# Optimization experiments

Hardware: AMD Instinct MI355X
Metric: run time of the kernel (lower is better)

## Reference

```python
import jax, jax.numpy as jnp
import numpy as np

N_ATOMS = 51200
N_MOL = 512
FEAT = 384


def setup_inputs() -> dict:
    key = jax.random.key(0)
    ks = jax.random.split(key, 20)
    s = 0.05  # small random weights instead of the degenerate zero-init
    inp = {
        "node_feats": jax.random.normal(ks[0], (N_ATOMS, FEAT), jnp.float32),
        "energy": jax.random.normal(ks[1], (N_MOL,), jnp.float32),
        "forces": jax.random.normal(ks[2], (N_ATOMS, 3), jnp.float32),
        "stress": jax.random.normal(ks[3], (N_MOL, 3, 3), jnp.float32),
        "W1": jax.random.normal(ks[4], (64, 256), jnp.float32) * s,
        "b1": jnp.zeros((64,), jnp.float32),
        "W2": jax.random.normal(ks[5], (16, 64), jnp.float32) * s,
        "b2": jnp.zeros((16,), jnp.float32),
        "W3": jax.random.normal(ks[6], (1, 16), jnp.float32) * s,
        "b3": jnp.zeros((1,), jnp.float32),
        "W1f": jax.random.normal(ks[7], (64, 256), jnp.float32) * s,
        "b1f": jnp.zeros((64,), jnp.float32),
        "W2f": jax.random.normal(ks[8], (16, 64), jnp.float32) * s,
        "b2f": jnp.zeros((16,), jnp.float32),
        "W3f": jax.random.normal(ks[9], (1, 16), jnp.float32) * s,
        "b3f": jnp.zeros((1,), jnp.float32),
        "S_uncert": jnp.zeros((1,), jnp.float32),
        # atom -> molecule segment ids (sorted, every molecule non-empty)
        "batch_idx": jnp.repeat(jnp.arange(N_MOL, dtype=jnp.int64), N_ATOMS // N_MOL),
    }
    return inp


def _mlp(x, W1, b1, W2, b2, W3, b3):
    h = jax.nn.silu(x @ W1.T + b1)
    h = jax.nn.silu(h @ W2.T + b2)
    return h @ W3.T + b3  # [N, 1]


def reference(node_feats, energy, forces, stress,
              W1, b1, W2, b2, W3, b3,
              W1f, b1f, W2f, b2f, W3f, b3f,
              S_uncert, batch_idx):
    # concat first 128 and last 128 feature channels -> [N, 256]
    nf = jnp.concatenate([node_feats[:, :128], node_feats[:, -128:]], axis=1)

    # E head: faithfully zeroed out and replaced by constant 0.6
    e_stds = jnp.exp(_mlp(nf, W1, b1, W2, b2, W3, b3))[:, 0] * 0 + 0.6  # [N]
    # F head
    f_u = jnp.exp(_mlp(nf, W1f, b1f, W2f, b2f, W3f, b3f))[:, 0] * 0.1   # [N]
    force_uncert = jnp.stack([f_u, f_u, f_u], axis=-1)                  # [N, 3]
    # stress uncert: constant 0.1/16 (S_uncert term zeroed, kept faithfully)
    stress_uncert = jnp.ones_like(stress) * jnp.exp(S_uncert[0]) * 0 + 0.1 / 16

    # per-molecule mean of e_stds via segment sums (scatter_add in torch)
    eu_sum = jax.ops.segment_sum(e_stds, batch_idx, num_segments=N_MOL)
    n_atoms = jax.ops.segment_sum(jnp.ones_like(e_stds), batch_idx, num_segments=N_MOL)
    energy_uncert = eu_sum / n_atoms  # [n_mol]

    return (energy, forces, stress, energy_uncert, force_uncert, stress_uncert)
```

## Files before the change

kernel.cpp:

```cpp
#include <hip/hip_runtime.h>
#include <hip/hip_bf16.h>

#define N_ATOMS 51200

#define OUT_FUNC 159232

typedef __attribute__((ext_vector_type(4))) float f32x4;
typedef __attribute__((ext_vector_type(2))) unsigned u32x2;
typedef __attribute__((ext_vector_type(4))) unsigned u32x4;
typedef __attribute__((ext_vector_type(8))) short s16x8;

constexpr int BLK = 256;

__device__ __forceinline__ unsigned pack2(float lo, float hi) {
    return __builtin_amdgcn_perm(__float_as_uint(hi), __float_as_uint(lo), 0x07060302);
}
__device__ __forceinline__ s16x8 pack8(f32x4 lo, f32x4 hi) {
    union { u32x4 u; s16x8 s; } c;
    c.u.x = pack2(lo.x, lo.y); c.u.y = pack2(lo.z, lo.w);
    c.u.z = pack2(hi.x, hi.y); c.u.w = pack2(hi.z, hi.w);
    return c.s;
}
__device__ __forceinline__ short bftrunc(float x) {
    return (short)(__float_as_uint(x) >> 16);
}
__device__ __forceinline__ float silu_(float v) { return v / (1.0f + __expf(-v)); }

__global__ __launch_bounds__(BLK, 4) void funcert_kernel(
    const float* __restrict__ nf,
    const float* __restrict__ energy,
    const float* __restrict__ forces,
    const float* __restrict__ stress,
    const float* __restrict__ W1f, const float* __restrict__ b1f,
    const float* __restrict__ W2f, const float* __restrict__ b2f,
    const float* __restrict__ W3f, const float* __restrict__ b3f,
    float* __restrict__ out)
{
    const int t   = threadIdx.x;
    const int gid = blockIdx.x * BLK + t;

    __shared__ short Xq[2][64 * 64];
    __shared__ short H1s[64 * 64];

    const int lane  = t & 63;
    const int w     = t >> 6;
    const int g     = lane >> 4;
    const int col   = lane & 15;
    const int abase = blockIdx.x * 64;
    const int ch    = w * 16 + col;

    const int rb  = t >> 4;
    const int f4c = t & 15;
    const float4* nfr = (const float4*)nf + (size_t)(abase + rb) * 96 + f4c;
    const int wbyte0 = rb * 128 + (f4c & 1) * 8;

    #define XQ_ISSUE(dst, qb)                                            \
        { _Pragma("unroll")                                              \
          for (int i = 0; i < 4; ++i)                                    \
              dst[i] = *(const f32x4*)(nfr + (size_t)i * 16 * 96 + (qb)); }

    #define XQ_STASH(buf, src)                                           \
        { _Pragma("unroll")                                              \
          for (int i = 0; i < 4; ++i) {                                  \
              const int r = rb + 16 * i;                                 \
              u32x2 bb;                                                  \
              bb.x = pack2(src[i].x, src[i].y);                          \
              bb.y = pack2(src[i].z, src[i].w);                          \
              *(u32x2*)((char*)(buf) + (wbyte0 + 2048 * i +              \
                        ((((f4c >> 1) ^ (r & 7))) << 4))) = bb;          \
          } }

    #define WQ_ISSUE(dst, q)                                             \
        { _Pragma("unroll")                                              \
          for (int ks2 = 0; ks2 < 2; ++ks2) {                            \
              const float* p = W1f + ch * 256 + (q) * 64 + ks2 * 32 + g * 8; \
              dst[2 * ks2]     = *(const f32x4*)p;                       \
              dst[2 * ks2 + 1] = *(const f32x4*)(p + 4);                 \
          } }

    #define Q_COMPUTE(buf, wf)                                           \
        { _Pragma("unroll")                                              \
          for (int mt = 0; mt < 4; ++mt) {                               \
              const int row = mt * 16 + col;                             \
              _Pragma("unroll")                                          \
              for (int ks2 = 0; ks2 < 2; ++ks2) {                        \
                  const int sl = (ks2 * 4 + g) ^ (row & 7);              \
                  const s16x8 af = *(const s16x8*)((buf) + row * 64 + sl * 8); \
                  acc[mt] = __builtin_amdgcn_mfma_f32_16x16x32_bf16(af, wf[ks2], acc[mt], 0, 0, 0); \
              } } }

    f32x4 cv = {0.f, 0.f, 0.f, 0.f}; int co = -1;
    if (gid < 40960) {
        co = gid;
        if      (gid < 128)   { cv = ((const f32x4*)energy)[gid]; }
        else if (gid < 38528) { cv = ((const f32x4*)forces)[gid - 128]; }
        else if (gid < 39680) { cv = ((const f32x4*)stress)[gid - 38528]; }
        else if (gid < 39808) { cv = (f32x4){0.6f, 0.6f, 0.6f, 0.6f}; }
        else { cv = (f32x4){0.00625f, 0.00625f, 0.00625f, 0.00625f}; co = gid + 38400; }
    }

    f32x4 wv[4];
    WQ_ISSUE(wv, 0);
    const float b1v = b1f[ch];
    f32x4 xa[4], xb[4], xc[4];
    XQ_ISSUE(xa, 0);
    XQ_ISSUE(xb, 16);
    XQ_ISSUE(xc, 64);

    f32x4 acc[4];
    #pragma unroll
    for (int mt = 0; mt < 4; ++mt) acc[mt] = (f32x4){0.f, 0.f, 0.f, 0.f};
    s16x8 wf[2];

    wf[0] = pack8(wv[0], wv[1]); wf[1] = pack8(wv[2], wv[3]);
    XQ_STASH(Xq[0], xa);
    __syncthreads();
    WQ_ISSUE(wv, 1);
    XQ_ISSUE(xa, 80);
    Q_COMPUTE(Xq[0], wf);
    __syncthreads();

    wf[0] = pack8(wv[0], wv[1]); wf[1] = pack8(wv[2], wv[3]);
    XQ_STASH(Xq[1], xb);
    __syncthreads();
    WQ_ISSUE(wv, 2);
    Q_COMPUTE(Xq[1], wf);
    __syncthreads();

    wf[0] = pack8(wv[0], wv[1]); wf[1] = pack8(wv[2], wv[3]);
    XQ_STASH(Xq[0], xc);
    __syncthreads();
    WQ_ISSUE(wv, 3);
    Q_COMPUTE(Xq[0], wf);
    __syncthreads();

    wf[0] = pack8(wv[0], wv[1]); wf[1] = pack8(wv[2], wv[3]);
    XQ_STASH(Xq[1], xa);
    __syncthreads();
    Q_COMPUTE(Xq[1], wf);

    #pragma unroll
    for (int mt = 0; mt < 4; ++mt) {
        #pragma unroll
        for (int r = 0; r < 4; ++r) {
            const int atom = mt * 16 + g * 4 + r;
            H1s[atom * 64 + ch] = bftrunc(silu_(acc[mt][r] + b1v));
        }
    }
    __syncthreads();

    s16x8 w2frag[2];
    #pragma unroll
    for (int ks = 0; ks < 2; ++ks) {
        const float* p = W2f + col * 64 + ks * 32 + g * 8;
        w2frag[ks] = pack8(*(const f32x4*)p, *(const f32x4*)(p + 4));
    }
    const int arow = w * 16 + col;
    f32x4 a2 = {0.f, 0.f, 0.f, 0.f};
    #pragma unroll
    for (int ks = 0; ks < 2; ++ks) {
        const s16x8 af = *(const s16x8*)(H1s + arow * 64 + ks * 32 + g * 8);
        a2 = __builtin_amdgcn_mfma_f32_16x16x32_bf16(af, w2frag[ks], a2, 0, 0, 0);
    }

    const float b2v = b2f[col];
    const float w3v = W3f[col];
    float y[4];
    #pragma unroll
    for (int r = 0; r < 4; ++r)
        y[r] = silu_(a2[r] + b2v) * w3v;
    #pragma unroll
    for (int m = 1; m < 16; m <<= 1) {
        #pragma unroll
        for (int r = 0; r < 4; ++r)
            y[r] += __shfl_xor(y[r], m, 64);
    }
    const float b3v = b3f[0];
    float fu[4];
    #pragma unroll
    for (int r = 0; r < 4; ++r)
        fu[r] = __expf(y[r] + b3v) * 0.1f;

    if (col < 12) {
        const int a_ = col / 3, c = col - a_ * 3;
        const float v = (a_ == 0) ? fu[0] : (a_ == 1) ? fu[1] : (a_ == 2) ? fu[2] : fu[3];
        const int atom = w * 16 + g * 4 + a_;
        out[OUT_FUNC + 3 * (abase + atom) + c] = v;
    }

    if (co >= 0) ((f32x4*)out)[co] = cv;
}

extern "C" void kernel_launch(void* const* d_in, const int* in_sizes, int n_in,
                              void* d_out, int out_size, void* d_ws, size_t ws_size,
                              hipStream_t stream) {
    const float* nf     = (const float*)d_in[0];
    const float* energy = (const float*)d_in[1];
    const float* forces = (const float*)d_in[2];
    const float* stress = (const float*)d_in[3];
    const float* W1f    = (const float*)d_in[10];
    const float* b1f    = (const float*)d_in[11];
    const float* W2f    = (const float*)d_in[12];
    const float* b2f    = (const float*)d_in[13];
    const float* W3f    = (const float*)d_in[14];
    const float* b3f    = (const float*)d_in[15];
    float* out = (float*)d_out;

    dim3 grid(N_ATOMS / 64);
    funcert_kernel<<<grid, BLK, 0, stream>>>(nf, energy, forces, stress,
                                             W1f, b1f, W2f, b2f, W3f, b3f, out);
}
```

Measured before the change: 20.69 us.

## Stage node features into LDS via direct global_load_lds in fp32

Replaces the register-staged path for node feature tiles with asynchronous global-to-LDS loads. Before, tiles were loaded to registers, packed to bf16 and stored to LDS. The tiles now stay fp32 in LDS, in an XOR-swizzled layout, and are converted to bf16 only when building MFMA operands. This removes the intermediate registers and one barrier per stage, reducing VGPR pressure and instruction count. The cost is a doubled LDS footprint for the double buffer and a shallower prefetch, which may limit occupancy or latency hiding.

```diff
diff --git a/kernel.cpp b/kernel.cpp
--- a/kernel.cpp
+++ b/kernel.cpp
@@ -6,7 +6,6 @@
 #define OUT_FUNC 159232
 
 typedef __attribute__((ext_vector_type(4))) float f32x4;
-typedef __attribute__((ext_vector_type(2))) unsigned u32x2;
 typedef __attribute__((ext_vector_type(4))) unsigned u32x4;
 typedef __attribute__((ext_vector_type(8))) short s16x8;
 
@@ -39,7 +38,7 @@
     const int t   = threadIdx.x;
     const int gid = blockIdx.x * BLK + t;
 
-    __shared__ short Xq[2][64 * 64];
+    __shared__ float Xq[2][64 * 64];
     __shared__ short H1s[64 * 64];
 
     const int lane  = t & 63;
@@ -49,44 +48,43 @@
     const int abase = blockIdx.x * 64;
     const int ch    = w * 16 + col;
 
-    const int rb  = t >> 4;
-    const int f4c = t & 15;
-    const float4* nfr = (const float4*)nf + (size_t)(abase + rb) * 96 + f4c;
-    const int wbyte0 = rb * 128 + (f4c & 1) * 8;
-
-    #define XQ_ISSUE(dst, qb)                                            \
-        { _Pragma("unroll")                                              \
-          for (int i = 0; i < 4; ++i)                                    \
-              dst[i] = *(const f32x4*)(nfr + (size_t)i * 16 * 96 + (qb)); }
-
-    #define XQ_STASH(buf, src)                                           \
-        { _Pragma("unroll")                                              \
-          for (int i = 0; i < 4; ++i) {                                  \
-              const int r = rb + 16 * i;                                 \
-              u32x2 bb;                                                  \
-              bb.x = pack2(src[i].x, src[i].y);                          \
-              bb.y = pack2(src[i].z, src[i].w);                          \
-              *(u32x2*)((char*)(buf) + (wbyte0 + 2048 * i +              \
-                        ((((f4c >> 1) ^ (r & 7))) << 4))) = bb;          \
+    const int rloc = lane >> 4;
+    const int sl   = lane & 15;
+
+    #define GLD_Q(b, qf)                                                     \
+        { _Pragma("unroll")                                                  \
+          for (int i2 = 0; i2 < 4; ++i2) {                                   \
+              const int ii = w * 4 + i2;                                     \
+              const int r  = 4 * ii + rloc;                                  \
+              const int c  = sl ^ ((r & 7) << 1);                            \
+              const float* src = nf + (size_t)(abase + r) * 384 + (qf) + c * 4; \
+              __builtin_amdgcn_global_load_lds(                              \
+                  (const __attribute__((address_space(1))) void*)src,        \
+                  (__attribute__((address_space(3))) void*)(&Xq[b][ii * 256]), \
+                  16, 0, 0);                                                 \
           } }
 
-    #define WQ_ISSUE(dst, q)                                             \
-        { _Pragma("unroll")                                              \
-          for (int ks2 = 0; ks2 < 2; ++ks2) {                            \
+    #define WQ_ISSUE(dst, q)                                                 \
+        { _Pragma("unroll")                                                  \
+          for (int ks2 = 0; ks2 < 2; ++ks2) {                                \
               const float* p = W1f + ch * 256 + (q) * 64 + ks2 * 32 + g * 8; \
-              dst[2 * ks2]     = *(const f32x4*)p;                       \
-              dst[2 * ks2 + 1] = *(const f32x4*)(p + 4);                 \
+              dst[2 * ks2]     = *(const f32x4*)p;                           \
+              dst[2 * ks2 + 1] = *(const f32x4*)(p + 4);                     \
           } }
 
-    #define Q_COMPUTE(buf, wf)                                           \
-        { _Pragma("unroll")                                              \
-          for (int mt = 0; mt < 4; ++mt) {                               \
-              const int row = mt * 16 + col;                             \
-              _Pragma("unroll")                                          \
-              for (int ks2 = 0; ks2 < 2; ++ks2) {                        \
-                  const int sl = (ks2 * 4 + g) ^ (row & 7);              \
-                  const s16x8 af = *(const s16x8*)((buf) + row * 64 + sl * 8); \
-                  acc[mt] = __builtin_amdgcn_mfma_f32_16x16x32_bf16(af, wf[ks2], acc[mt], 0, 0, 0); \
+    #define Q_COMPUTE(b, wfv)                                                \
+        { _Pragma("unroll")                                                  \
+          for (int mt = 0; mt < 4; ++mt) {                                   \
+              const int row = mt * 16 + col;                                 \
+              const int xr  = (row & 7) << 1;                                \
+              _Pragma("unroll")                                              \
+              for (int ks2 = 0; ks2 < 2; ++ks2) {                            \
+                  const int s0 = ((ks2 << 3) + (g << 1)) ^ xr;               \
+                  const float* p = &Xq[b][row * 64 + s0 * 4];                \
+                  const f32x4 lo = *(const f32x4*)p;                         \
+                  const f32x4 hi = *(const f32x4*)(p + 4);                   \
+                  acc[mt] = __builtin_amdgcn_mfma_f32_16x16x32_bf16(         \
+                              pack8(lo, hi), wfv[ks2], acc[mt], 0, 0, 0);    \
               } } }
 
     f32x4 cv = {0.f, 0.f, 0.f, 0.f}; int co = -1;
@@ -102,42 +100,35 @@
     f32x4 wv[4];
     WQ_ISSUE(wv, 0);
     const float b1v = b1f[ch];
-    f32x4 xa[4], xb[4], xc[4];
-    XQ_ISSUE(xa, 0);
-    XQ_ISSUE(xb, 16);
-    XQ_ISSUE(xc, 64);
+    GLD_Q(0, 0);
+
+    s16x8 wf[2];
+    wf[0] = pack8(wv[0], wv[1]); wf[1] = pack8(wv[2], wv[3]);
 
     f32x4 acc[4];
     #pragma unroll
     for (int mt = 0; mt < 4; ++mt) acc[mt] = (f32x4){0.f, 0.f, 0.f, 0.f};
-    s16x8 wf[2];
-
-    wf[0] = pack8(wv[0], wv[1]); wf[1] = pack8(wv[2], wv[3]);
-    XQ_STASH(Xq[0], xa);
+
     __syncthreads();
     WQ_ISSUE(wv, 1);
-    XQ_ISSUE(xa, 80);
-    Q_COMPUTE(Xq[0], wf);
-    __syncthreads();
-
-    wf[0] = pack8(wv[0], wv[1]); wf[1] = pack8(wv[2], wv[3]);
-    XQ_STASH(Xq[1], xb);
-    __syncthreads();
+    GLD_Q(1, 64);
+    Q_COMPUTE(0, wf);
+    __syncthreads();
+
+    wf[0] = pack8(wv[0], wv[1]); wf[1] = pack8(wv[2], wv[3]);
     WQ_ISSUE(wv, 2);
-    Q_COMPUTE(Xq[1], wf);
-    __syncthreads();
-
-    wf[0] = pack8(wv[0], wv[1]); wf[1] = pack8(wv[2], wv[3]);
-    XQ_STASH(Xq[0], xc);
-    __syncthreads();
+    GLD_Q(0, 256);
+    Q_COMPUTE(1, wf);
+    __syncthreads();
+
+    wf[0] = pack8(wv[0], wv[1]); wf[1] = pack8(wv[2], wv[3]);
     WQ_ISSUE(wv, 3);
-    Q_COMPUTE(Xq[0], wf);
-    __syncthreads();
-
-    wf[0] = pack8(wv[0], wv[1]); wf[1] = pack8(wv[2], wv[3]);
-    XQ_STASH(Xq[1], xa);
-    __syncthreads();
-    Q_COMPUTE(Xq[1], wf);
+    GLD_Q(1, 320);
+    Q_COMPUTE(0, wf);
+    __syncthreads();
+
+    wf[0] = pack8(wv[0], wv[1]); wf[1] = pack8(wv[2], wv[3]);
+    Q_COMPUTE(1, wf);
 
     #pragma unroll
     for (int mt = 0; mt < 4; ++mt) {
```

After: 21.30 us. +3.0%, slower.

## Restructure layer-1 pipeline with two-deep prefetch and single raw barriers

Applied to the files above, without the earlier changes.

Splits the shared staging buffer into two named buffers and prefetches two quarters of both weights and node features at a time, instead of one weight quarter plus three feature quarters. Each stage now uses one LDS-count wait plus one raw s_barrier instead of two __syncthreads. The aim is to cut barrier count and keep more global loads in flight. Occupancy is raised to 5 blocks per CU through launch bounds. The risks are register spills under the tighter bound and a write-after-read hazard on the reused buffers, which here relies on the single barrier between the stages that touch each buffer.

```diff
diff --git a/kernel.cpp b/kernel.cpp
--- a/kernel.cpp
+++ b/kernel.cpp
@@ -26,7 +26,10 @@
 }
 __device__ __forceinline__ float silu_(float v) { return v / (1.0f + __expf(-v)); }
 
-__global__ __launch_bounds__(BLK, 4) void funcert_kernel(
+#define LGKM0()   asm volatile("s_waitcnt lgkmcnt(0)" ::: "memory")
+#define RAWBAR()  asm volatile("s_barrier" ::: "memory")
+
+__global__ __launch_bounds__(BLK, 5) void funcert_kernel(
     const float* __restrict__ nf,
     const float* __restrict__ energy,
     const float* __restrict__ forces,
@@ -39,7 +42,8 @@
     const int t   = threadIdx.x;
     const int gid = blockIdx.x * BLK + t;
 
-    __shared__ short Xq[2][64 * 64];
+    __shared__ short Xq0[64 * 64];
+    __shared__ short Xq1[64 * 64];
     __shared__ short H1s[64 * 64];
 
     const int lane  = t & 63;
@@ -78,7 +82,7 @@
               dst[2 * ks2 + 1] = *(const f32x4*)(p + 4);                 \
           } }
 
-    #define Q_COMPUTE(buf, wf)                                           \
+    #define Q_COMPUTE(buf, wfv)                                          \
         { _Pragma("unroll")                                              \
           for (int mt = 0; mt < 4; ++mt) {                               \
               const int row = mt * 16 + col;                             \
@@ -86,7 +90,7 @@
               for (int ks2 = 0; ks2 < 2; ++ks2) {                        \
                   const int sl = (ks2 * 4 + g) ^ (row & 7);              \
                   const s16x8 af = *(const s16x8*)((buf) + row * 64 + sl * 8); \
-                  acc[mt] = __builtin_amdgcn_mfma_f32_16x16x32_bf16(af, wf[ks2], acc[mt], 0, 0, 0); \
+                  acc[mt] = __builtin_amdgcn_mfma_f32_16x16x32_bf16(af, wfv[ks2], acc[mt], 0, 0, 0); \
               } } }
 
     f32x4 cv = {0.f, 0.f, 0.f, 0.f}; int co = -1;
@@ -99,45 +103,41 @@
         else { cv = (f32x4){0.00625f, 0.00625f, 0.00625f, 0.00625f}; co = gid + 38400; }
     }
 
-    f32x4 wv[4];
-    WQ_ISSUE(wv, 0);
+    f32x4 wv0[4], wv1[4], x0[4], x1[4];
+    WQ_ISSUE(wv0, 0);
+    XQ_ISSUE(x0, 0);
+    WQ_ISSUE(wv1, 1);
+    XQ_ISSUE(x1, 16);
     const float b1v = b1f[ch];
-    f32x4 xa[4], xb[4], xc[4];
-    XQ_ISSUE(xa, 0);
-    XQ_ISSUE(xb, 16);
-    XQ_ISSUE(xc, 64);
 
     f32x4 acc[4];
     #pragma unroll
     for (int mt = 0; mt < 4; ++mt) acc[mt] = (f32x4){0.f, 0.f, 0.f, 0.f};
     s16x8 wf[2];
 
-    wf[0] = pack8(wv[0], wv[1]); wf[1] = pack8(wv[2], wv[3]);
-    XQ_STASH(Xq[0], xa);
-    __syncthreads();
-    WQ_ISSUE(wv, 1);
-    XQ_ISSUE(xa, 80);
-    Q_COMPUTE(Xq[0], wf);
-    __syncthreads();
-
-    wf[0] = pack8(wv[0], wv[1]); wf[1] = pack8(wv[2], wv[3]);
-    XQ_STASH(Xq[1], xb);
-    __syncthreads();
-    WQ_ISSUE(wv, 2);
-    Q_COMPUTE(Xq[1], wf);
-    __syncthreads();
-
-    wf[0] = pack8(wv[0], wv[1]); wf[1] = pack8(wv[2], wv[3]);
-    XQ_STASH(Xq[0], xc);
-    __syncthreads();
-    WQ_ISSUE(wv, 3);
-    Q_COMPUTE(Xq[0], wf);
-    __syncthreads();
-
-    wf[0] = pack8(wv[0], wv[1]); wf[1] = pack8(wv[2], wv[3]);
-    XQ_STASH(Xq[1], xa);
-    __syncthreads();
-    Q_COMPUTE(Xq[1], wf);
+    wf[0] = pack8(wv0[0], wv0[1]); wf[1] = pack8(wv0[2], wv0[3]);
+    XQ_STASH(Xq0, x0);
+    WQ_ISSUE(wv0, 2);
+    XQ_ISSUE(x0, 64);
+    LGKM0(); RAWBAR();
+    Q_COMPUTE(Xq0, wf);
+
+    wf[0] = pack8(wv1[0], wv1[1]); wf[1] = pack8(wv1[2], wv1[3]);
+    XQ_STASH(Xq1, x1);
+    WQ_ISSUE(wv1, 3);
+    XQ_ISSUE(x1, 80);
+    LGKM0(); RAWBAR();
+    Q_COMPUTE(Xq1, wf);
+
+    wf[0] = pack8(wv0[0], wv0[1]); wf[1] = pack8(wv0[2], wv0[3]);
+    XQ_STASH(Xq0, x0);
+    LGKM0(); RAWBAR();
+    Q_COMPUTE(Xq0, wf);
+
+    wf[0] = pack8(wv1[0], wv1[1]); wf[1] = pack8(wv1[2], wv1[3]);
+    XQ_STASH(Xq1, x1);
+    LGKM0(); RAWBAR();
+    Q_COMPUTE(Xq1, wf);
 
     #pragma unroll
     for (int mt = 0; mt < 4; ++mt) {
```

Result: slower. 27.31 us (+32.0%).
